# Performance work log

Hardware: AMD Instinct MI355X
Metric: run time of the kernel (lower is better)

The kernel has to match this reference:

```python
import jax, jax.numpy as jnp
import numpy as np

HEAD_COUNT = 8  # matches init_kwargs head_count

def _branch(q_in, k_in, v_in, Wq, bq, Wk, bk, Wv, bv):
    # q_in/k_in/v_in: [B, N, D]. Linear (efficient) attention, per-head.
    B, N, D = q_in.shape
    H = HEAD_COUNT
    hd = D // H
    q = q_in @ Wq + bq            # [B, N, D]
    k = k_in @ Wk + bk
    v = v_in @ Wv + bv
    # permute(0,2,1) then contiguous channel slices per head == [B,H,hd,N]
    q = q.reshape(B, N, H, hd).transpose(0, 2, 3, 1)  # [B,H,hd,Nq]
    k = k.reshape(B, N, H, hd).transpose(0, 2, 3, 1)  # [B,H,hd,Nk]
    v = v.reshape(B, N, H, hd).transpose(0, 2, 3, 1)  # [B,H,hd,Nk]
    q = jax.nn.softmax(q, axis=3)  # softmax over sequence positions (torch dim=2)
    k = jax.nn.softmax(k, axis=2)  # softmax over head channels (torch dim=1)
    # context = k @ v^T : [B,H,hd_c,hd_d]
    ctx = jnp.einsum('bhcn,bhdn->bhcd', k, v)
    # attended = context^T @ q : [B,H,hd_d,Nq]
    att = jnp.einsum('bhcd,bhcn->bhdn', ctx, q)
    # concat heads along channel dim, then transpose -> [B, Nq, D]
    return att.reshape(B, D, N).transpose(0, 2, 1)

def setup_inputs() -> dict:
    key = jax.random.key(0)
    ks = jax.random.split(key, 16)
    B, N, D = 4, 8192, 256
    s = 0.02
    inp = {
        'f1': jax.random.normal(ks[0], (B, N, D), jnp.float32),
        'f2': jax.random.normal(ks[1], (B, N, D), jnp.float32),
        'f3': jax.random.normal(ks[2], (B, N, D), jnp.float32),
        'f4': jax.random.normal(ks[3], (B, N, D), jnp.float32),
        'f1_pos_embed': jax.random.normal(ks[4], (B, N, D), jnp.float32),
        'f2_pos_embed': jax.random.normal(ks[5], (B, N, D), jnp.float32),
        'f3_pos_embed': jax.random.normal(ks[6], (B, N, D), jnp.float32),
        'f4_pos_embed': jax.random.normal(ks[7], (B, N, D), jnp.float32),
        'Wq': jax.random.normal(ks[8], (3, D, D), jnp.float32) * s,
        'bq': jax.random.normal(ks[9], (3, D), jnp.float32) * s,
        'Wk': jax.random.normal(ks[10], (3, D, D), jnp.float32) * s,
        'bk': jax.random.normal(ks[11], (3, D), jnp.float32) * s,
        'Wv': jax.random.normal(ks[12], (3, D, D), jnp.float32) * s,
        'bv': jax.random.normal(ks[13], (3, D), jnp.float32) * s,
        'Wrp': jax.random.normal(ks[14], (3 * D, D), jnp.float32) * s,
        'brp': jax.random.normal(ks[15], (D,), jnp.float32) * s,
    }
    return inp

def reference(f1, f2, f3, f4, f1_pos_embed, f2_pos_embed, f3_pos_embed, f4_pos_embed,
              Wq, bq, Wk, bk, Wv, bv, Wrp, brp):
    q_in = f1 + f1_pos_embed
    agg21 = _branch(q_in, f2 + f2_pos_embed, f2, Wq[0], bq[0], Wk[0], bk[0], Wv[0], bv[0])
    agg31 = _branch(q_in, f3 + f3_pos_embed, f3, Wq[1], bq[1], Wk[1], bk[1], Wv[1], bv[1])
    agg41 = _branch(q_in, f4 + f4_pos_embed, f4, Wq[2], bq[2], Wk[2], bk[2], Wv[2], bv[2])
    out = jnp.concatenate([agg21, agg31, agg41], axis=-1)  # [B, N, 3D]
    return out @ Wrp + brp  # dropout p=0.0 -> identity
```

## Files before the change

### kernel.cpp

```cpp
#include <hip/hip_runtime.h>
#include <hip/hip_bf16.h>

typedef __attribute__((ext_vector_type(8))) short short8;
typedef __attribute__((ext_vector_type(4))) short shortx4;
typedef __attribute__((ext_vector_type(4))) float floatx4;
typedef __attribute__((ext_vector_type(16))) float floatx16;

#define N_SEQ 8192
#define M_ROWS 32768

__device__ __forceinline__ unsigned short f2bf(float f) {
    unsigned int x = __builtin_bit_cast(unsigned int, f);
    x += 0x7fff + ((x >> 16) & 1);
    return (unsigned short)(x >> 16);
}

__global__ __launch_bounds__(256) void transpose_w(
    const float* __restrict__ Wq, const float* __restrict__ Wk,
    const float* __restrict__ Wv, unsigned short* __restrict__ Wt)
{
    __shared__ unsigned short tile[64][72];
    int job = blockIdx.x;
    int tt = blockIdx.y;
    int k0 = (tt >> 2) * 64, n0 = (tt & 3) * 64;
    const float* src =
        (job < 3) ? (Wq + job * 65536) :
        (job < 6) ? (Wk + (job - 3) * 65536) :
                    (Wv + (job - 6) * 65536);
    int tid = threadIdx.x;
    {
        int r = tid >> 2, cs = (tid & 3) * 16;
        const float* s = src + (size_t)(k0 + r) * 256 + n0 + cs;
        #pragma unroll
        for (int h = 0; h < 2; h++) {
            float4 x0 = *(const float4*)(s + h * 8);
            float4 x1 = *(const float4*)(s + h * 8 + 4);
            short8 v;
            v[0] = (short)f2bf(x0.x); v[1] = (short)f2bf(x0.y);
            v[2] = (short)f2bf(x0.z); v[3] = (short)f2bf(x0.w);
            v[4] = (short)f2bf(x1.x); v[5] = (short)f2bf(x1.y);
            v[6] = (short)f2bf(x1.z); v[7] = (short)f2bf(x1.w);
            *(short8*)&tile[r][cs + h * 8] = v;
        }
    }
    __syncthreads();
    {
        int rn = tid >> 2, ks = (tid & 3) * 16;
        unsigned short tmp[16];
        #pragma unroll
        for (int q = 0; q < 16; q++) tmp[q] = tile[ks + q][rn];
        short8 v0, v1;
        #pragma unroll
        for (int q = 0; q < 8; q++) { v0[q] = (short)tmp[q]; v1[q] = (short)tmp[q + 8]; }
        unsigned short* dst = Wt + (size_t)job * 65536 + (size_t)(n0 + rn) * 256 + k0 + ks;
        *(short8*)dst = v0;
        *(short8*)(dst + 8) = v1;
    }
}

__global__ __launch_bounds__(256) void projq_kernel(
    const float* __restrict__ f1, const float* __restrict__ p1,
    const float* __restrict__ bq, const unsigned short* __restrict__ Wt,
    unsigned short* __restrict__ expQ, float* __restrict__ S)
{
    __shared__ __align__(16) unsigned short As[64][264];
    int m0 = blockIdx.x * 64;
    int b = m0 >> 13;
    int tid = threadIdx.x;
    int lane = tid & 63, wave = tid >> 6;
    int wm = wave >> 1, wn = wave & 1;
    int quad = lane >> 4, l15 = lane & 15;

    {
        int row = tid >> 2, seg = tid & 3;
        const float* fr = f1 + (size_t)(m0 + row) * 256 + seg * 64;
        const float* pr = p1 + (size_t)(m0 + row) * 256 + seg * 64;
        #pragma unroll
        for (int q = 0; q < 8; q++) {
            float4 x0 = *(const float4*)(fr + q * 8);
            float4 x1 = *(const float4*)(fr + q * 8 + 4);
            float4 y0 = *(const float4*)(pr + q * 8);
            float4 y1 = *(const float4*)(pr + q * 8 + 4);
            short8 v;
            v[0] = (short)f2bf(x0.x + y0.x); v[1] = (short)f2bf(x0.y + y0.y);
            v[2] = (short)f2bf(x0.z + y0.z); v[3] = (short)f2bf(x0.w + y0.w);
            v[4] = (short)f2bf(x1.x + y1.x); v[5] = (short)f2bf(x1.y + y1.y);
            v[6] = (short)f2bf(x1.z + y1.z); v[7] = (short)f2bf(x1.w + y1.w);
            *(short8*)&As[row][seg * 64 + q * 8] = v;
        }
    }
    __syncthreads();

    for (int nj = 0; nj < 6; nj++) {
        int j = nj >> 1;
        int n0 = (nj & 1) * 128;
        const unsigned short* Wj = Wt + (size_t)j * 65536;

        floatx4 acc[2][4];
        #pragma unroll
        for (int sm = 0; sm < 2; sm++)
            #pragma unroll
            for (int sn = 0; sn < 4; sn++)
                #pragma unroll
                for (int r = 0; r < 4; r++) acc[sm][sn][r] = 0.0f;

        #pragma unroll
        for (int ks = 0; ks < 8; ks++) {
            short8 af[2], bfr[4];
            #pragma unroll
            for (int sm = 0; sm < 2; sm++)
                af[sm] = *(const short8*)&As[wm * 32 + sm * 16 + l15][ks * 32 + quad * 8];
            #pragma unroll
            for (int sn = 0; sn < 4; sn++) {
                int ncol = n0 + wn * 64 + sn * 16 + l15;
                bfr[sn] = *(const short8*)(Wj + (size_t)ncol * 256 + ks * 32 + quad * 8);
            }
            #pragma unroll
            for (int sm = 0; sm < 2; sm++)
                #pragma unroll
                for (int sn = 0; sn < 4; sn++)
                    acc[sm][sn] = __builtin_amdgcn_mfma_f32_16x16x32_bf16(
                        af[sm], bfr[sn], acc[sm][sn], 0, 0, 0);
        }

        float colsum[4] = {0.f, 0.f, 0.f, 0.f};
        #pragma unroll
        for (int sm = 0; sm < 2; sm++)
            #pragma unroll
            for (int sn = 0; sn < 4; sn++) {
                float bb = bq[j * 256 + n0 + wn * 64 + sn * 16 + l15];
                #pragma unroll
                for (int r = 0; r < 4; r++) {
                    float e = __expf(acc[sm][sn][r] + bb);
                    colsum[sn] += e;
                    int row = m0 + wm * 32 + sm * 16 + quad * 4 + r;
                    int col = j * 256 + n0 + wn * 64 + sn * 16 + l15;
                    expQ[(size_t)row * 768 + col] = f2bf(e);
                }
            }
        #pragma unroll
        for (int sn = 0; sn < 4; sn++) {
            float v = colsum[sn];
            v += __shfl_xor(v, 16, 64);
            v += __shfl_xor(v, 32, 64);
            if (quad == 0)
                atomicAdd(&S[b * 768 + j * 256 + n0 + wn * 64 + sn * 16 + l15], v);
        }
    }
}

__device__ __forceinline__ void pf_issue(
    int tau, int srow, int seg,
    const float* f2, const float* f3, const float* f4,
    const float* p2, const float* p3, const float* p4,
    float4 (&pf)[16])
{
    int ib = tau >> 7;
    int b = ib & 3, i = ib >> 2;
    const float* fb = ((i == 0) ? f2 : (i == 1) ? f3 : f4) + (size_t)b * N_SEQ * 256;
    const float* pb = ((i == 0) ? p2 : (i == 1) ? p3 : p4) + (size_t)b * N_SEQ * 256;
    const float* fr = fb + (size_t)((tau & 127) * 64 + srow) * 256;
    const float* pr = pb + (size_t)((tau & 127) * 64 + srow) * 256;
    #pragma unroll
    for (int q = 0; q < 4; q++) {
        int c0 = q * 64 + seg * 8;
        pf[q * 4 + 0] = *(const float4*)(fr + c0);
        pf[q * 4 + 1] = *(const float4*)(fr + c0 + 4);
        pf[q * 4 + 2] = *(const float4*)(pr + c0);
        pf[q * 4 + 3] = *(const float4*)(pr + c0 + 4);
    }
}

__global__ __launch_bounds__(512, 4) void projkv_ctx(
    const float* __restrict__ f2, const float* __restrict__ f3, const float* __restrict__ f4,
    const float* __restrict__ p2, const float* __restrict__ p3, const float* __restrict__ p4,
    const float* __restrict__ bk, const float* __restrict__ bv,
    const unsigned short* __restrict__ Wt, float* __restrict__ ctx)
{
    __shared__ __align__(16) unsigned short sh[36864];

    int tid = threadIdx.x;
    int lane = tid & 63, wn = tid >> 6;
    int quad = lane >> 4, l15 = lane & 15;
    int srow = tid >> 3, seg = tid & 7;

    int gbase = -1;
    int cur_ib = -1;
    const unsigned short *Wk_ = nullptr, *Wv_ = nullptr;
    float bkk[2] = {0.f, 0.f}, bvv[2] = {0.f, 0.f};
    floatx16 ctxacc;
    float4 pf[16];

    pf_issue(blockIdx.x * 3, srow, seg, f2, f3, f4, p2, p3, p4, pf);

    for (int j = 0; j < 3; j++) {
        int tau = blockIdx.x * 3 + j;
        int ib = tau >> 7;
        if (ib != cur_ib) {
            if (gbase >= 0) {
                int d = lane & 31;
                #pragma unroll
                for (int reg = 0; reg < 16; reg++) {
                    int cc = (reg & 3) + 8 * (reg >> 2) + 4 * (lane >> 5);
                    atomicAdd(&ctx[(size_t)gbase * 1024 + cc * 32 + d], ctxacc[reg]);
                }
            }
            cur_ib = ib;
            int b = ib & 3, i = ib >> 2;
            Wk_ = Wt + (size_t)(3 + i) * 65536;
            Wv_ = Wt + (size_t)(6 + i) * 65536;
            #pragma unroll
            for (int sn = 0; sn < 2; sn++) {
                bkk[sn] = bk[i * 256 + wn * 32 + sn * 16 + l15];
                bvv[sn] = bv[i * 256 + wn * 32 + sn * 16 + l15];
            }
            gbase = i * 32 + b * 8 + wn;
            #pragma unroll
            for (int q = 0; q < 16; q++) ctxacc[q] = 0.0f;
        }

        __syncthreads();
        {
            #pragma unroll
            for (int q = 0; q < 4; q++) {
                int c0 = q * 64 + seg * 8;
                float4 x0 = pf[q * 4 + 0];
                float4 x1 = pf[q * 4 + 1];
                float4 y0 = pf[q * 4 + 2];
                float4 y1 = pf[q * 4 + 3];
                short8 vv, kk;
                vv[0] = (short)f2bf(x0.x); kk[0] = (short)f2bf(x0.x + y0.x);
                vv[1] = (short)f2bf(x0.y); kk[1] = (short)f2bf(x0.y + y0.y);
                vv[2] = (short)f2bf(x0.z); kk[2] = (short)f2bf(x0.z + y0.z);
                vv[3] = (short)f2bf(x0.w); kk[3] = (short)f2bf(x0.w + y0.w);
                vv[4] = (short)f2bf(x1.x); kk[4] = (short)f2bf(x1.x + y1.x);
                vv[5] = (short)f2bf(x1.y); kk[5] = (short)f2bf(x1.y + y1.y);
                vv[6] = (short)f2bf(x1.z); kk[6] = (short)f2bf(x1.z + y1.z);
                vv[7] = (short)f2bf(x1.w); kk[7] = (short)f2bf(x1.w + y1.w);
                *(short8*)&sh[srow * 264 + c0] = kk;
                *(short8*)&sh[18432 + srow * 264 + c0] = vv;
            }
        }
        __syncthreads();

        floatx4 acc[4][2];
        #pragma unroll
        for (int sm = 0; sm < 4; sm++)
            #pragma unroll
            for (int sn = 0; sn < 2; sn++)
                #pragma unroll
                for (int r = 0; r < 4; r++) acc[sm][sn][r] = 0.0f;
        #pragma unroll
        for (int ks = 0; ks < 8; ks++) {
            short8 af[4], bfr[2];
            #pragma unroll
            for (int sm = 0; sm < 4; sm++)
                af[sm] = *(const short8*)&sh[(sm * 16 + l15) * 264 + ks * 32 + quad * 8];
            #pragma unroll
            for (int sn = 0; sn < 2; sn++) {
                int ncol = wn * 32 + sn * 16 + l15;
                bfr[sn] = *(const short8*)(Wk_ + (size_t)ncol * 256 + ks * 32 + quad * 8);
            }
            #pragma unroll
            for (int sm = 0; sm < 4; sm++)
                #pragma unroll
                for (int sn = 0; sn < 2; sn++)
                    acc[sm][sn] = __builtin_amdgcn_mfma_f32_16x16x32_bf16(
                        af[sm], bfr[sn], acc[sm][sn], 0, 0, 0);
        }
        #pragma unroll
        for (int sm = 0; sm < 4; sm++)
            #pragma unroll
            for (int r = 0; r < 4; r++) {
                float e0 = __expf(acc[sm][0][r] + bkk[0]);
                float e1 = __expf(acc[sm][1][r] + bkk[1]);
                float t = e0 + e1;
                t += __shfl_xor(t, 1, 64);
                t += __shfl_xor(t, 2, 64);
                t += __shfl_xor(t, 4, 64);
                t += __shfl_xor(t, 8, 64);
                float inv = 1.0f / t;
                acc[sm][0][r] = e0 * inv;
                acc[sm][1][r] = e1 * inv;
            }
        __syncthreads();
        #pragma unroll
        for (int sm = 0; sm < 4; sm++)
            #pragma unroll
            for (int sn = 0; sn < 2; sn++) {
                shortx4 v;
                #pragma unroll
                for (int r = 0; r < 4; r++) v[r] = (short)f2bf(acc[sm][sn][r]);
                *(shortx4*)&sh[(wn * 32 + sn * 16 + l15) * 72 + sm * 16 + quad * 4] = v;
            }

        #pragma unroll
        for (int sm = 0; sm < 4; sm++)
            #pragma unroll
            for (int sn = 0; sn < 2; sn++)
                #pragma unroll
                for (int r = 0; r < 4; r++) acc[sm][sn][r] = 0.0f;
        #pragma unroll
        for (int ks = 0; ks < 8; ks++) {
            short8 af[4], bfr[2];
            #pragma unroll
            for (int sm = 0; sm < 4; sm++)
                af[sm] = *(const short8*)&sh[18432 + (sm * 16 + l15) * 264 + ks * 32 + quad * 8];
            #pragma unroll
            for (int sn = 0; sn < 2; sn++) {
                int ncol = wn * 32 + sn * 16 + l15;
                bfr[sn] = *(const short8*)(Wv_ + (size_t)ncol * 256 + ks * 32 + quad * 8);
            }
            #pragma unroll
            for (int sm = 0; sm < 4; sm++)
                #pragma unroll
                for (int sn = 0; sn < 2; sn++)
                    acc[sm][sn] = __builtin_amdgcn_mfma_f32_16x16x32_bf16(
                        af[sm], bfr[sn], acc[sm][sn], 0, 0, 0);
        }
        __syncthreads();
        #pragma unroll
        for (int sm = 0; sm < 4; sm++)
            #pragma unroll
            for (int sn = 0; sn < 2; sn++) {
                shortx4 v;
                #pragma unroll
                for (int r = 0; r < 4; r++) v[r] = (short)f2bf(acc[sm][sn][r] + bvv[sn]);
                *(shortx4*)&sh[18432 + (wn * 32 + sn * 16 + l15) * 72 + sm * 16 + quad * 4] = v;
            }

        if (j < 2)
            pf_issue(tau + 1, srow, seg, f2, f3, f4, p2, p3, p4, pf);

        {
            int hc = wn * 32 + (lane & 31);
            int nb = (lane >> 5) * 8;
            #pragma unroll
            for (int s = 0; s < 4; s++) {
                short8 afr  = *(const short8*)&sh[hc * 72 + s * 16 + nb];
                short8 bfr2 = *(const short8*)&sh[18432 + hc * 72 + s * 16 + nb];
                ctxacc = __builtin_amdgcn_mfma_f32_32x32x16_bf16(afr, bfr2, ctxacc, 0, 0, 0);
            }
        }
    }

    if (gbase >= 0) {
        int d = lane & 31;
        #pragma unroll
        for (int reg = 0; reg < 16; reg++) {
            int cc = (reg & 3) + 8 * (reg >> 2) + 4 * (lane >> 5);
            atomicAdd(&ctx[(size_t)gbase * 1024 + cc * 32 + d], ctxacc[reg]);
        }
    }
}

__global__ __launch_bounds__(256) void wtilde_kernel(
    const float* __restrict__ ctx, const float* __restrict__ S,
    const float* __restrict__ Wrp, unsigned short* __restrict__ Wtld)
{
    __shared__ float cp[1024];
    int g = blockIdx.x;
    int i = g >> 5, b = (g >> 3) & 3, h = g & 7;
    int t = threadIdx.x;
    #pragma unroll
    for (int q = 0; q < 4; q++) {
        int idx = t + q * 256;
        int c = idx >> 5;
        cp[idx] = ctx[(size_t)g * 1024 + idx] / S[b * 768 + i * 256 + h * 32 + c];
    }
    __syncthreads();
    float accv[32];
    #pragma unroll
    for (int c = 0; c < 32; c++) accv[c] = 0.0f;
    for (int d = 0; d < 32; d++) {
        float w = Wrp[(size_t)(i * 256 + h * 32 + d) * 256 + t];
        #pragma unroll
        for (int c = 0; c < 32; c++) accv[c] += cp[c * 32 + d] * w;
    }
    for (int c = 0; c < 32; c++)
        Wtld[((size_t)b * 256 + t) * 768 + i * 256 + h * 32 + c] = f2bf(accv[c]);
}

__global__ __launch_bounds__(256) void out_kernel(
    const unsigned short* __restrict__ expQ, const unsigned short* __restrict__ Wtld,
    const float* __restrict__ brp, float* __restrict__ outp)
{
    __shared__ __align__(16) unsigned short As[128][72];
    int m0 = blockIdx.x * 128;
    int n0 = blockIdx.y * 128;
    int b = m0 >> 13;
    const unsigned short* Wb = Wtld + (size_t)b * 256 * 768;
    int tid = threadIdx.x;
    int lane = tid & 63, wave = tid >> 6;
    int wm = wave >> 1, wn = wave & 1;
    int quad = lane >> 4, l15 = lane & 15;

    floatx4 acc[4][4];
    #pragma unroll
    for (int a = 0; a < 4; a++)
        #pragma unroll
        for (int cc = 0; cc < 4; cc++)
            #pragma unroll
            for (int r = 0; r < 4; r++) acc[a][cc][r] = 0.0f;

    for (int kt = 0; kt < 12; kt++) {
        __syncthreads();
        #pragma unroll
        for (int p = 0; p < 4; p++) {
            int r = (tid >> 3) + p * 32;
            int kc = (tid & 7) * 8;
            size_t ga = (size_t)(m0 + r) * 768 + kt * 64 + kc;
            *(short8*)&As[r][kc] = *(const short8*)(expQ + ga);
        }
        __syncthreads();
        #pragma unroll
        for (int kc = 0; kc < 64; kc += 32) {
            short8 af[4], bfr[4];
            #pragma unroll
            for (int sm = 0; sm < 4; sm++)
                af[sm] = *(const short8*)&As[wm * 64 + sm * 16 + l15][kc + quad * 8];
            #pragma unroll
            for (int sn = 0; sn < 4; sn++) {
                int ncol = n0 + wn * 64 + sn * 16 + l15;
                bfr[sn] = *(const short8*)(Wb + (size_t)ncol * 768 + kt * 64 + kc + quad * 8);
            }
            #pragma unroll
            for (int sm = 0; sm < 4; sm++)
                #pragma unroll
                for (int sn = 0; sn < 4; sn++)
                    acc[sm][sn] = __builtin_amdgcn_mfma_f32_16x16x32_bf16(
                        af[sm], bfr[sn], acc[sm][sn], 0, 0, 0);
        }
    }

    float bb[4];
    #pragma unroll
    for (int sn = 0; sn < 4; sn++) bb[sn] = brp[n0 + wn * 64 + sn * 16 + l15];
    #pragma unroll
    for (int sm = 0; sm < 4; sm++)
        #pragma unroll
        for (int sn = 0; sn < 4; sn++)
            #pragma unroll
            for (int r = 0; r < 4; r++) {
                int row = m0 + wm * 64 + sm * 16 + quad * 4 + r;
                int col = n0 + wn * 64 + sn * 16 + l15;
                outp[(size_t)row * 256 + col] = acc[sm][sn][r] + bb[sn];
            }
}

extern "C" void kernel_launch(void* const* d_in, const int* in_sizes, int n_in,
                              void* d_out, int out_size, void* d_ws, size_t ws_size,
                              hipStream_t stream)
{
    (void)in_sizes; (void)n_in; (void)out_size; (void)ws_size;
    const float* f1  = (const float*)d_in[0];
    const float* f2  = (const float*)d_in[1];
    const float* f3  = (const float*)d_in[2];
    const float* f4  = (const float*)d_in[3];
    const float* p1  = (const float*)d_in[4];
    const float* p2  = (const float*)d_in[5];
    const float* p3  = (const float*)d_in[6];
    const float* p4  = (const float*)d_in[7];
    const float* Wq  = (const float*)d_in[8];
    const float* bq  = (const float*)d_in[9];
    const float* Wk  = (const float*)d_in[10];
    const float* bk  = (const float*)d_in[11];
    const float* Wv  = (const float*)d_in[12];
    const float* bv  = (const float*)d_in[13];
    const float* Wrp = (const float*)d_in[14];
    const float* brp = (const float*)d_in[15];

    char* ws = (char*)d_ws;
    unsigned short* expQ = (unsigned short*)(ws);
    unsigned short* Wt   = (unsigned short*)(ws + 50331648);
    unsigned short* Wtld = (unsigned short*)(ws + 51511296);
    float*          ctx  = (float*)(ws + 53084160);
    float*          S    = (float*)(ws + 53477376);

    hipMemsetAsync(ctx, 0, 393216 + 12288, stream);

    transpose_w<<<dim3(9, 16), 256, 0, stream>>>(Wq, Wk, Wv, Wt);
    projq_kernel<<<dim3(512), 256, 0, stream>>>(f1, p1, bq, Wt, expQ, S);
    projkv_ctx<<<dim3(512), 512, 0, stream>>>(f2, f3, f4, p2, p3, p4, bk, bv, Wt, ctx);
    wtilde_kernel<<<dim3(96), 256, 0, stream>>>(ctx, S, Wrp, Wtld);
    out_kernel<<<dim3(256, 2), 256, 0, stream>>>(expQ, Wtld, brp, (float*)d_out);
}
```

Baseline: 465.4 us.

## Double-buffer out_kernel A tiles and drop register prefetch in projkv_ctx

In out_kernel, the shared-memory A tile is double-buffered. The next K-slice is loaded from global into registers while the MFMAs run on the current buffer, which leaves one barrier per iteration instead of two. In projkv_ctx, the cross-iteration register prefetch of f/pos inputs is removed and replaced with direct loads at the start of each tile, which lowers register pressure but exposes global load latency. Net effect depends on which kernel dominates and whether occupancy improves in projkv_ctx.

```diff
diff --git a/kernel.cpp b/kernel.cpp
--- a/kernel.cpp
+++ b/kernel.cpp
@@ -149,28 +149,6 @@
     }
 }
 
-__device__ __forceinline__ void pf_issue(
-    int tau, int srow, int seg,
-    const float* f2, const float* f3, const float* f4,
-    const float* p2, const float* p3, const float* p4,
-    float4 (&pf)[16])
-{
-    int ib = tau >> 7;
-    int b = ib & 3, i = ib >> 2;
-    const float* fb = ((i == 0) ? f2 : (i == 1) ? f3 : f4) + (size_t)b * N_SEQ * 256;
-    const float* pb = ((i == 0) ? p2 : (i == 1) ? p3 : p4) + (size_t)b * N_SEQ * 256;
-    const float* fr = fb + (size_t)((tau & 127) * 64 + srow) * 256;
-    const float* pr = pb + (size_t)((tau & 127) * 64 + srow) * 256;
-    #pragma unroll
-    for (int q = 0; q < 4; q++) {
-        int c0 = q * 64 + seg * 8;
-        pf[q * 4 + 0] = *(const float4*)(fr + c0);
-        pf[q * 4 + 1] = *(const float4*)(fr + c0 + 4);
-        pf[q * 4 + 2] = *(const float4*)(pr + c0);
-        pf[q * 4 + 3] = *(const float4*)(pr + c0 + 4);
-    }
-}
-
 __global__ __launch_bounds__(512, 4) void projkv_ctx(
     const float* __restrict__ f2, const float* __restrict__ f3, const float* __restrict__ f4,
     const float* __restrict__ p2, const float* __restrict__ p3, const float* __restrict__ p4,
@@ -186,12 +164,10 @@
 
     int gbase = -1;
     int cur_ib = -1;
+    const float *fin = nullptr, *pin = nullptr;
     const unsigned short *Wk_ = nullptr, *Wv_ = nullptr;
     float bkk[2] = {0.f, 0.f}, bvv[2] = {0.f, 0.f};
     floatx16 ctxacc;
-    float4 pf[16];
-
-    pf_issue(blockIdx.x * 3, srow, seg, f2, f3, f4, p2, p3, p4, pf);
 
     for (int j = 0; j < 3; j++) {
         int tau = blockIdx.x * 3 + j;
@@ -207,6 +183,8 @@
             }
             cur_ib = ib;
             int b = ib & 3, i = ib >> 2;
+            fin = ((i == 0) ? f2 : (i == 1) ? f3 : f4) + (size_t)b * N_SEQ * 256;
+            pin = ((i == 0) ? p2 : (i == 1) ? p3 : p4) + (size_t)b * N_SEQ * 256;
             Wk_ = Wt + (size_t)(3 + i) * 65536;
             Wv_ = Wt + (size_t)(6 + i) * 65536;
             #pragma unroll
@@ -218,16 +196,19 @@
             #pragma unroll
             for (int q = 0; q < 16; q++) ctxacc[q] = 0.0f;
         }
+        int m0 = (tau & 127) * 64;
 
         __syncthreads();
         {
+            const float* fr = fin + (size_t)(m0 + srow) * 256;
+            const float* pr = pin + (size_t)(m0 + srow) * 256;
             #pragma unroll
             for (int q = 0; q < 4; q++) {
                 int c0 = q * 64 + seg * 8;
-                float4 x0 = pf[q * 4 + 0];
-                float4 x1 = pf[q * 4 + 1];
-                float4 y0 = pf[q * 4 + 2];
-                float4 y1 = pf[q * 4 + 3];
+                float4 x0 = *(const float4*)(fr + c0);
+                float4 x1 = *(const float4*)(fr + c0 + 4);
+                float4 y0 = *(const float4*)(pr + c0);
+                float4 y1 = *(const float4*)(pr + c0 + 4);
                 short8 vv, kk;
                 vv[0] = (short)f2bf(x0.x); kk[0] = (short)f2bf(x0.x + y0.x);
                 vv[1] = (short)f2bf(x0.y); kk[1] = (short)f2bf(x0.y + y0.y);
@@ -329,9 +310,6 @@
                 *(shortx4*)&sh[18432 + (wn * 32 + sn * 16 + l15) * 72 + sm * 16 + quad * 4] = v;
             }
 
-        if (j < 2)
-            pf_issue(tau + 1, srow, seg, f2, f3, f4, p2, p3, p4, pf);
-
         {
             int hc = wn * 32 + (lane & 31);
             int nb = (lane >> 5) * 8;
@@ -385,7 +363,7 @@
     const unsigned short* __restrict__ expQ, const unsigned short* __restrict__ Wtld,
     const float* __restrict__ brp, float* __restrict__ outp)
 {
-    __shared__ __align__(16) unsigned short As[128][72];
+    __shared__ __align__(16) unsigned short As[2][128][72];
     int m0 = blockIdx.x * 128;
     int n0 = blockIdx.y * 128;
     int b = m0 >> 13;
@@ -394,6 +372,7 @@
     int lane = tid & 63, wave = tid >> 6;
     int wm = wave >> 1, wn = wave & 1;
     int quad = lane >> 4, l15 = lane & 15;
+    int sr = tid >> 3, skc = (tid & 7) * 8;
 
     floatx4 acc[4][4];
     #pragma unroll
@@ -403,22 +382,35 @@
             #pragma unroll
             for (int r = 0; r < 4; r++) acc[a][cc][r] = 0.0f;
 
+    {
+        short8 st0, st1, st2, st3;
+        st0 = *(const short8*)(expQ + (size_t)(m0 + sr +  0) * 768 + skc);
+        st1 = *(const short8*)(expQ + (size_t)(m0 + sr + 32) * 768 + skc);
+        st2 = *(const short8*)(expQ + (size_t)(m0 + sr + 64) * 768 + skc);
+        st3 = *(const short8*)(expQ + (size_t)(m0 + sr + 96) * 768 + skc);
+        *(short8*)&As[0][sr +  0][skc] = st0;
+        *(short8*)&As[0][sr + 32][skc] = st1;
+        *(short8*)&As[0][sr + 64][skc] = st2;
+        *(short8*)&As[0][sr + 96][skc] = st3;
+    }
+    __syncthreads();
+
+    int cur = 0;
     for (int kt = 0; kt < 12; kt++) {
-        __syncthreads();
-        #pragma unroll
-        for (int p = 0; p < 4; p++) {
-            int r = (tid >> 3) + p * 32;
-            int kc = (tid & 7) * 8;
-            size_t ga = (size_t)(m0 + r) * 768 + kt * 64 + kc;
-            *(short8*)&As[r][kc] = *(const short8*)(expQ + ga);
-        }
-        __syncthreads();
+        short8 st0, st1, st2, st3;
+        if (kt < 11) {
+            size_t kb = (size_t)(kt + 1) * 64 + skc;
+            st0 = *(const short8*)(expQ + (size_t)(m0 + sr +  0) * 768 + kb);
+            st1 = *(const short8*)(expQ + (size_t)(m0 + sr + 32) * 768 + kb);
+            st2 = *(const short8*)(expQ + (size_t)(m0 + sr + 64) * 768 + kb);
+            st3 = *(const short8*)(expQ + (size_t)(m0 + sr + 96) * 768 + kb);
+        }
         #pragma unroll
         for (int kc = 0; kc < 64; kc += 32) {
             short8 af[4], bfr[4];
             #pragma unroll
             for (int sm = 0; sm < 4; sm++)
-                af[sm] = *(const short8*)&As[wm * 64 + sm * 16 + l15][kc + quad * 8];
+                af[sm] = *(const short8*)&As[cur][wm * 64 + sm * 16 + l15][kc + quad * 8];
             #pragma unroll
             for (int sn = 0; sn < 4; sn++) {
                 int ncol = n0 + wn * 64 + sn * 16 + l15;
@@ -430,6 +422,15 @@
                 for (int sn = 0; sn < 4; sn++)
                     acc[sm][sn] = __builtin_amdgcn_mfma_f32_16x16x32_bf16(
                         af[sm], bfr[sn], acc[sm][sn], 0, 0, 0);
+        }
+        if (kt < 11) {
+            int nxt = cur ^ 1;
+            *(short8*)&As[nxt][sr +  0][skc] = st0;
+            *(short8*)&As[nxt][sr + 32][skc] = st1;
+            *(short8*)&As[nxt][sr + 64][skc] = st2;
+            *(short8*)&As[nxt][sr + 96][skc] = st3;
+            __syncthreads();
+            cur = nxt;
         }
     }
 
```

Result: faster. 430.8 us (-7.4%).
